# Kernel optimization log

Hardware: AMD Instinct MI355X
Metric: run time of the kernel (lower is better)

The kernel has to match this reference:

```python
import jax, jax.numpy as jnp
import numpy as np

HIDDEN = 2048
NUM_HEADS = 32
NUM_KV_HEADS = 8
HEAD_DIM = 64
ROPE_THETA = 10000.0


def _rope_tables(S, dtype=jnp.float32):
    freqs = 1.0 / (ROPE_THETA ** (jnp.arange(0, HEAD_DIM, 2, dtype=jnp.float32) / HEAD_DIM))
    angles = jnp.arange(S, dtype=jnp.float32)[:, None] * freqs[None, :]  # [S, D/2]
    return jnp.cos(angles).astype(dtype), jnp.sin(angles).astype(dtype)


def _apply_rope(x, cos, sin):
    # x: [B, H, S, D] with interleaved even/odd rotation pairs
    xe = x[..., 0::2]
    xo = x[..., 1::2]
    oe = xe * cos - xo * sin
    oo = xe * sin + xo * cos
    return jnp.stack([oe, oo], axis=-1).reshape(x.shape)


def setup_inputs() -> dict:
    key = jax.random.key(0)
    ks = jax.random.split(key, 5)
    scale = 0.02
    return {
        "x": jax.random.normal(ks[0], (2, 2048, HIDDEN), dtype=jnp.float32),
        "wq": jax.random.normal(ks[1], (NUM_HEADS * HEAD_DIM, HIDDEN), dtype=jnp.float32) * scale,
        "wk": jax.random.normal(ks[2], (NUM_KV_HEADS * HEAD_DIM, HIDDEN), dtype=jnp.float32) * scale,
        "wv": jax.random.normal(ks[3], (NUM_KV_HEADS * HEAD_DIM, HIDDEN), dtype=jnp.float32) * scale,
        "wo": jax.random.normal(ks[4], (HIDDEN, NUM_HEADS * HEAD_DIM), dtype=jnp.float32) * scale,
    }


def reference(x, wq, wk, wv, wo):
    B, S, _ = x.shape
    G = NUM_HEADS // NUM_KV_HEADS  # GQA group size

    q = (x @ wq.T).reshape(B, S, NUM_HEADS, HEAD_DIM).transpose(0, 2, 1, 3)      # [B,Hq,S,D]
    k = (x @ wk.T).reshape(B, S, NUM_KV_HEADS, HEAD_DIM).transpose(0, 2, 1, 3)   # [B,Hkv,S,D]
    v = (x @ wv.T).reshape(B, S, NUM_KV_HEADS, HEAD_DIM).transpose(0, 2, 1, 3)

    cos, sin = _rope_tables(S, x.dtype)
    q = _apply_rope(q, cos, sin)
    k = _apply_rope(k, cos, sin)

    # GQA without materializing repeated K/V: fold group dim into q
    qg = q.reshape(B, NUM_KV_HEADS, G, S, HEAD_DIM)
    scale = 1.0 / jnp.sqrt(jnp.asarray(HEAD_DIM, dtype=x.dtype))
    scores = jnp.einsum("bkgsd,bktd->bkgst", qg, k) * scale  # [B,Hkv,G,S,S]

    causal = jnp.tril(jnp.ones((S, S), dtype=bool))
    scores = jnp.where(causal, scores, jnp.finfo(scores.dtype).min)
    probs = jax.nn.softmax(scores, axis=-1)

    out = jnp.einsum("bkgst,bktd->bkgsd", probs, v)                 # [B,Hkv,G,S,D]
    out = out.reshape(B, NUM_HEADS, S, HEAD_DIM).transpose(0, 2, 1, 3).reshape(B, S, NUM_HEADS * HEAD_DIM)
    return out @ wo.T
```

## Files before the change

kernel.cpp:

```cpp
#include <hip/hip_runtime.h>
#include <hip/hip_bf16.h>

typedef __hip_bfloat16 bf16;
typedef __attribute__((ext_vector_type(8))) short short8;
typedef __attribute__((ext_vector_type(4))) float f32x4;

#define S_LEN 2048
#define BATCH 2
#define M_TOT 4096
#define HID 2048
#define NH 32
#define NKV 8
#define HD 64
#define KVD 512
#define QSCALE 0.125f

#define MFMA16(a, b, c) __builtin_amdgcn_mfma_f32_16x16x32_bf16(a, b, c, 0, 0, 0)

__device__ __forceinline__ void gload_lds16(const bf16* g, bf16* l) {
    __builtin_amdgcn_global_load_lds((const __attribute__((address_space(1))) void*)g,
                                     (__attribute__((address_space(3))) void*)l,
                                     16, 0, 0);
}

__device__ __forceinline__ float b2f(short v) {
    unsigned u = ((unsigned)(unsigned short)v) << 16;
    float f; __builtin_memcpy(&f, &u, 4); return f;
}

#define N8_X   1048576
#define N8_WQ   524288
#define N8_WK   131072
#define N8_TOT 2359296
__global__ void cast_all_kernel(const float* __restrict__ x, const float* __restrict__ wq,
                                const float* __restrict__ wk, const float* __restrict__ wv,
                                const float* __restrict__ wo, bf16* __restrict__ dst) {
    int stride = gridDim.x * blockDim.x;
    for (int i = blockIdx.x * blockDim.x + threadIdx.x; i < N8_TOT; i += stride) {
        const float* s; int off;
        if (i < N8_X)                        { s = x;  off = i; }
        else if (i < N8_X + N8_WQ)           { s = wq; off = i - N8_X; }
        else if (i < N8_X + N8_WQ + N8_WK)   { s = wk; off = i - (N8_X + N8_WQ); }
        else if (i < N8_X + N8_WQ + 2*N8_WK) { s = wv; off = i - (N8_X + N8_WQ + N8_WK); }
        else                                 { s = wo; off = i - (N8_X + N8_WQ + 2*N8_WK); }
        const float4* sp = (const float4*)(s + (size_t)off * 8);
        float4 a = sp[0], b = sp[1];
        bf16 tmp[8];
        tmp[0] = __float2bfloat16(a.x); tmp[1] = __float2bfloat16(a.y);
        tmp[2] = __float2bfloat16(a.z); tmp[3] = __float2bfloat16(a.w);
        tmp[4] = __float2bfloat16(b.x); tmp[5] = __float2bfloat16(b.y);
        tmp[6] = __float2bfloat16(b.z); tmp[7] = __float2bfloat16(b.w);
        *(short8*)(dst + (size_t)i * 8) = *(short8*)tmp;
    }
}

__global__ void rope_tables_kernel(float* __restrict__ cosb, float* __restrict__ sinb) {
    int idx = blockIdx.x * blockDim.x + threadIdx.x;
    if (idx >= S_LEN * 32) return;
    int s = idx >> 5, d = idx & 31;
    float freq = powf(10000.0f, -(float)(2 * d) / 64.0f);
    float ang = (float)s * freq;
    cosb[idx] = cosf(ang);
    sinb[idx] = sinf(ang);
}

__device__ __forceinline__ short8 rope8(short8 v, float4 c, float4 s, float scale) {
    short8 o;
    const float* cp = (const float*)&c;
    const float* sp = (const float*)&s;
    #pragma unroll
    for (int m = 0; m < 4; m++) {
        float xe = b2f(v[2 * m]) * scale;
        float xo = b2f(v[2 * m + 1]) * scale;
        bf16 oe = __float2bfloat16(xe * cp[m] - xo * sp[m]);
        bf16 oo = __float2bfloat16(xe * sp[m] + xo * cp[m]);
        short se, so;
        __builtin_memcpy(&se, &oe, 2); __builtin_memcpy(&so, &oo, 2);
        o[2 * m] = se; o[2 * m + 1] = so;
    }
    return o;
}

__device__ __forceinline__ void gemm_core(const bf16* __restrict__ A,
                                          const bf16* __restrict__ W,
                                          int K, int m0, int n0,
                                          bf16* As, bf16* Bs,
                                          f32x4 acc[4][4]) {
    int tid = threadIdx.x;
    int lane = tid & 63, wid = tid >> 6;
    int wr = wid >> 1, wc = wid & 1;
    int lhi = lane >> 4, llo = lane & 15;
    int c0 = tid, c1 = tid + 256;
    int r0 = c0 >> 2, s0 = ((c0 & 3) ^ ((r0 >> 1) & 3)) * 8;
    int r1 = c1 >> 2, s1 = ((c1 & 3) ^ ((r1 >> 1) & 3)) * 8;
    const bf16* gA0 = A + (size_t)(m0 + r0) * K + s0;
    const bf16* gA1 = A + (size_t)(m0 + r1) * K + s1;
    const bf16* gB0 = W + (size_t)(n0 + r0) * K + s0;
    const bf16* gB1 = W + (size_t)(n0 + r1) * K + s1;

    auto stage = [&](int buf, int k0) {
        bf16* a = As + buf * 4096;
        bf16* b = Bs + buf * 4096;
        gload_lds16(gA0 + k0, a + c0 * 8);
        gload_lds16(gA1 + k0, a + c1 * 8);
        gload_lds16(gB0 + k0, b + c0 * 8);
        gload_lds16(gB1 + k0, b + c1 * 8);
    };
    auto compute = [&](int buf) {
        const bf16* Ac = As + buf * 4096;
        const bf16* Bc = Bs + buf * 4096;
        short8 af[4], bfr[4];
        #pragma unroll
        for (int i = 0; i < 4; i++) {
            int row = wr * 64 + i * 16 + llo;
            af[i] = *(const short8*)(Ac + row * 32 + ((lhi ^ ((row >> 1) & 3)) * 8));
        }
        #pragma unroll
        for (int j = 0; j < 4; j++) {
            int row = wc * 64 + j * 16 + llo;
            bfr[j] = *(const short8*)(Bc + row * 32 + ((lhi ^ ((row >> 1) & 3)) * 8));
        }
        __builtin_amdgcn_s_setprio(1);
        #pragma unroll
        for (int i = 0; i < 4; i++)
            #pragma unroll
            for (int j = 0; j < 4; j++)
                acc[i][j] = MFMA16(af[i], bfr[j], acc[i][j]);
        __builtin_amdgcn_s_setprio(0);
    };

    int nt = K / 32;
    stage(0, 0);
    stage(1, 32);
    int b0 = 0, b1 = 1, b2 = 2;
    for (int t = 0; t < nt - 1; ++t) {
        asm volatile("s_waitcnt vmcnt(4)" ::: "memory");
        __builtin_amdgcn_s_barrier();
        if (t + 2 < nt) stage(b2, (t + 2) * 32);
        __builtin_amdgcn_sched_barrier(0);
        compute(b0);
        int tmp = b0; b0 = b1; b1 = b2; b2 = tmp;
    }
    asm volatile("s_waitcnt vmcnt(0)" ::: "memory");
    __builtin_amdgcn_s_barrier();
    compute(b0);
}

__global__ __launch_bounds__(256) void gemm_qkv_kernel(
        const bf16* __restrict__ xb,
        const bf16* __restrict__ wq, const bf16* __restrict__ wk, const bf16* __restrict__ wv,
        const float* __restrict__ cosb, const float* __restrict__ sinb,
        bf16* __restrict__ qb, bf16* __restrict__ kb, bf16* __restrict__ vtb) {
    __shared__ bf16 As[3 * 128 * 32];
    __shared__ bf16 Bs[3 * 128 * 32];
    int by = blockIdx.y;
    const bf16* W; bf16* Cb; int n0, ldc, mode;
    if (by < 16)      { W = wq; Cb = qb;  n0 = by * 128;        ldc = 2048; mode = 0; }
    else if (by < 20) { W = wk; Cb = kb;  n0 = (by - 16) * 128; ldc = 512;  mode = 2; }
    else              { W = wv; Cb = vtb; n0 = (by - 20) * 128; ldc = 0;    mode = 1; }
    int bx = blockIdx.x;
    int bxs = (bx & 7) * 4 + (bx >> 3);
    int m0 = bxs * 128;

    f32x4 acc[4][4] = {};
    gemm_core(xb, W, HID, m0, n0, As, Bs, acc);

    int lane = threadIdx.x & 63, wid = threadIdx.x >> 6;
    int wr = wid >> 1, wc = wid & 1;
    int lhi = lane >> 4, llo = lane & 15;
    #pragma unroll
    for (int i = 0; i < 4; i++)
        #pragma unroll
        for (int j = 0; j < 4; j++) {
            int col = wc * 64 + j * 16 + llo;
            #pragma unroll
            for (int r = 0; r < 4; r++) {
                int row = wr * 64 + i * 16 + lhi * 4 + r;
                int m = m0 + row;
                float v = acc[i][j][r];
                if (mode == 0) {
                    Cb[(size_t)m * ldc + n0 + col] = __float2bfloat16(v);
                } else if (mode == 1) {
                    int bb = m >> 11, ss = m & 2047;
                    Cb[((size_t)(bb * 512 + n0 + col)) * S_LEN + ss] = __float2bfloat16(v);
                } else {
                    int dcol = n0 + col;
                    int dd = dcol & 63;
                    int pidx = dd >> 1;
                    float sgn = (dd & 1) ? 1.0f : -1.0f;
                    int ss = m & 2047;
                    float c  = cosb[ss * 32 + pidx];
                    float sn = sinb[ss * 32 + pidx];
                    float o = __shfl_xor(v, 1, 64);
                    float outv = v * c + sgn * o * sn;
                    Cb[(size_t)m * 512 + dcol] = __float2bfloat16(outv);
                }
            }
        }
}

__global__ __launch_bounds__(256) void gemm_out_kernel(
        const bf16* __restrict__ attnb, const bf16* __restrict__ wob,
        float* __restrict__ out) {
    __shared__ bf16 As[3 * 128 * 32];
    __shared__ bf16 Bs[3 * 128 * 32];
    int bx = blockIdx.x;
    int bxs = (bx & 7) * 4 + (bx >> 3);
    int m0 = bxs * 128;
    int n0 = blockIdx.y * 128;
    f32x4 acc[4][4] = {};
    gemm_core(attnb, wob, HID, m0, n0, As, Bs, acc);

    int lane = threadIdx.x & 63, wid = threadIdx.x >> 6;
    int wr = wid >> 1, wc = wid & 1;
    int lhi = lane >> 4, llo = lane & 15;
    #pragma unroll
    for (int i = 0; i < 4; i++)
        #pragma unroll
        for (int j = 0; j < 4; j++) {
            int col = wc * 64 + j * 16 + llo;
            #pragma unroll
            for (int r = 0; r < 4; r++) {
                int row = wr * 64 + i * 16 + lhi * 4 + r;
                out[(size_t)(m0 + row) * HID + n0 + col] = acc[i][j][r];
            }
        }
}

__global__ __launch_bounds__(256, 4) void flash_kernel(
        const bf16* __restrict__ qb, const bf16* __restrict__ kb,
        const bf16* __restrict__ vtb, const float* __restrict__ cosb,
        const float* __restrict__ sinb, bf16* __restrict__ attnb) {
    __shared__ bf16 Ks[2][64 * 64];
    __shared__ bf16 Vs[2][64 * 64];
    __shared__ bf16 Pl[4][16 * 64];
    int bh = blockIdx.y;
    int b = bh >> 5, h = bh & 31;
    int kvh = h >> 2;
    int tid = threadIdx.x;
    int wid = tid >> 6, lane = tid & 63;
    int lhi = lane >> 4, llo = lane & 15;
    int jA = blockIdx.x, jB = 31 - jA;

    const bf16* Kg = kb + (size_t)(b * S_LEN) * KVD + kvh * HD;
    const bf16* Vg = vtb + (size_t)(b * 512 + kvh * 64) * S_LEN;

    int c0 = tid, c1 = tid + 256;
    int r0 = c0 >> 3, s0 = ((c0 & 7) ^ (r0 & 7)) * 8;
    int r1 = c1 >> 3, s1 = ((c1 & 7) ^ (r1 & 7)) * 8;

    bf16* pl = &Pl[wid][0];
    const int xw = llo & 7;
    const int hh = lhi >> 1;
    bf16* pwb = pl + llo * 64 + (lhi & 1) * 4;
    const int prd0 = llo * 64 + ((lhi ^ xw) * 8);
    const int prd1 = llo * 64 + (((lhi + 4) ^ xw) * 8);

    auto stage = [&](int buf, int t0) {
        gload_lds16(Kg + (size_t)(t0 + r0) * KVD + s0, &Ks[buf][c0 * 8]);
        gload_lds16(Kg + (size_t)(t0 + r1) * KVD + s1, &Ks[buf][c1 * 8]);
        gload_lds16(Vg + (size_t)r0 * S_LEN + t0 + s0, &Vs[buf][c0 * 8]);
        gload_lds16(Vg + (size_t)r1 * S_LEN + t0 + s1, &Vs[buf][c1 * 8]);
    };

    int qrowA0 = jA * 64 + wid * 16;
    int qrowB0 = jB * 64 + wid * 16;
    short8 qfA0, qfA1, qfB0, qfB1;
    {
        int spos = qrowA0 + llo;
        const bf16* qr = qb + ((size_t)(b * S_LEN) + spos) * (NH * HD) + h * HD;
        float4 c0v = *(const float4*)(cosb + spos * 32 + lhi * 4);
        float4 s0v = *(const float4*)(sinb + spos * 32 + lhi * 4);
        float4 c1v = *(const float4*)(cosb + spos * 32 + 16 + lhi * 4);
        float4 s1v = *(const float4*)(sinb + spos * 32 + 16 + lhi * 4);
        qfA0 = rope8(*(const short8*)(qr + lhi * 8), c0v, s0v, QSCALE);
        qfA1 = rope8(*(const short8*)(qr + 32 + lhi * 8), c1v, s1v, QSCALE);
    }
    {
        int spos = qrowB0 + llo;
        const bf16* qr = qb + ((size_t)(b * S_LEN) + spos) * (NH * HD) + h * HD;
        float4 c0v = *(const float4*)(cosb + spos * 32 + lhi * 4);
        float4 s0v = *(const float4*)(sinb + spos * 32 + lhi * 4);
        float4 c1v = *(const float4*)(cosb + spos * 32 + 16 + lhi * 4);
        float4 s1v = *(const float4*)(sinb + spos * 32 + 16 + lhi * 4);
        qfB0 = rope8(*(const short8*)(qr + lhi * 8), c0v, s0v, QSCALE);
        qfB1 = rope8(*(const short8*)(qr + 32 + lhi * 8), c1v, s1v, QSCALE);
    }

    f32x4 accA[4] = {}, accB[4] = {};
    float psumA = 0.f, psumB = 0.f;
    int qloc = wid * 16 + llo;

    stage(0, 0);
    asm volatile("s_waitcnt vmcnt(0)" ::: "memory");
    __builtin_amdgcn_s_barrier();
    int cur = 0;
    for (int t = 0; t <= jB; ++t) {
        int t0 = t * 64;
        if (t < jB) stage(cur ^ 1, t0 + 64);
        const bf16* Kc = &Ks[cur][0];
        const bf16* Vc = &Vs[cur][0];
        bool doA = (t <= jA);
        f32x4 zA[4], zB[4];
        __builtin_amdgcn_s_setprio(1);
        #pragma unroll
        for (int cb = 0; cb < 4; cb++) {
            int row = cb * 16 + llo;
            short8 k0 = *(const short8*)(Kc + row * 64 + ((lhi ^ xw) * 8));
            short8 k1 = *(const short8*)(Kc + row * 64 + (((lhi + 4) ^ xw) * 8));
            f32x4 zz = {0.f, 0.f, 0.f, 0.f};
            zz = MFMA16(k0, qfB0, zz);
            zz = MFMA16(k1, qfB1, zz);
            zB[cb] = zz;
            if (doA) {
                f32x4 yy = {0.f, 0.f, 0.f, 0.f};
                yy = MFMA16(k0, qfA0, yy);
                yy = MFMA16(k1, qfA1, yy);
                zA[cb] = yy;
            }
        }
        __builtin_amdgcn_s_setprio(0);
        if (doA) {
            bool diag = (t == jA);
            #pragma unroll
            for (int cb = 0; cb < 4; cb++) {
                float p0 = __expf(zA[cb][0]);
                float p1 = __expf(zA[cb][1]);
                float p2 = __expf(zA[cb][2]);
                float p3 = __expf(zA[cb][3]);
                if (diag) {
                    int kl = cb * 16 + lhi * 4;
                    p0 = (kl + 0 <= qloc) ? p0 : 0.f;
                    p1 = (kl + 1 <= qloc) ? p1 : 0.f;
                    p2 = (kl + 2 <= qloc) ? p2 : 0.f;
                    p3 = (kl + 3 <= qloc) ? p3 : 0.f;
                }
                psumA += (p0 + p1) + (p2 + p3);
                bf16 tmp[4];
                tmp[0] = __float2bfloat16(p0); tmp[1] = __float2bfloat16(p1);
                tmp[2] = __float2bfloat16(p2); tmp[3] = __float2bfloat16(p3);
                *(uint2*)(pwb + (((2 * cb + hh) ^ xw) * 8)) = *(uint2*)tmp;
            }
            short8 pa0 = *(const short8*)(pl + prd0);
            short8 pa1 = *(const short8*)(pl + prd1);
            __builtin_amdgcn_s_setprio(1);
            #pragma unroll
            for (int jb = 0; jb < 4; jb++) {
                int row = jb * 16 + llo;
                short8 v0 = *(const short8*)(Vc + row * 64 + ((lhi ^ xw) * 8));
                short8 v1 = *(const short8*)(Vc + row * 64 + (((lhi + 4) ^ xw) * 8));
                accA[jb] = MFMA16(pa0, v0, accA[jb]);
                accA[jb] = MFMA16(pa1, v1, accA[jb]);
            }
            __builtin_amdgcn_s_setprio(0);
        }
        {
            bool diag = (t == jB);
            #pragma unroll
            for (int cb = 0; cb < 4; cb++) {
                float p0 = __expf(zB[cb][0]);
                float p1 = __expf(zB[cb][1]);
                float p2 = __expf(zB[cb][2]);
                float p3 = __expf(zB[cb][3]);
                if (diag) {
                    int kl = cb * 16 + lhi * 4;
                    p0 = (kl + 0 <= qloc) ? p0 : 0.f;
                    p1 = (kl + 1 <= qloc) ? p1 : 0.f;
                    p2 = (kl + 2 <= qloc) ? p2 : 0.f;
                    p3 = (kl + 3 <= qloc) ? p3 : 0.f;
                }
                psumB += (p0 + p1) + (p2 + p3);
                bf16 tmp[4];
                tmp[0] = __float2bfloat16(p0); tmp[1] = __float2bfloat16(p1);
                tmp[2] = __float2bfloat16(p2); tmp[3] = __float2bfloat16(p3);
                *(uint2*)(pwb + (((2 * cb + hh) ^ xw) * 8)) = *(uint2*)tmp;
            }
            short8 pb0 = *(const short8*)(pl + prd0);
            short8 pb1 = *(const short8*)(pl + prd1);
            __builtin_amdgcn_s_setprio(1);
            #pragma unroll
            for (int jb = 0; jb < 4; jb++) {
                int row = jb * 16 + llo;
                short8 v0 = *(const short8*)(Vc + row * 64 + ((lhi ^ xw) * 8));
                short8 v1 = *(const short8*)(Vc + row * 64 + (((lhi + 4) ^ xw) * 8));
                accB[jb] = MFMA16(pb0, v0, accB[jb]);
                accB[jb] = MFMA16(pb1, v1, accB[jb]);
            }
            __builtin_amdgcn_s_setprio(0);
        }
        asm volatile("s_waitcnt vmcnt(0)" ::: "memory");
        __builtin_amdgcn_s_barrier();
        cur ^= 1;
    }
    psumA += __shfl_xor(psumA, 16, 64);
    psumA += __shfl_xor(psumA, 32, 64);
    psumB += __shfl_xor(psumB, 16, 64);
    psumB += __shfl_xor(psumB, 32, 64);
    float invA[4], invB[4];
    #pragma unroll
    for (int r = 0; r < 4; r++) {
        invA[r] = 1.0f / __shfl(psumA, lhi * 4 + r, 64);
        invB[r] = 1.0f / __shfl(psumB, lhi * 4 + r, 64);
    }
    size_t obaseA = ((size_t)(b * S_LEN) + qrowA0) * (NH * HD) + h * HD;
    size_t obaseB = ((size_t)(b * S_LEN) + qrowB0) * (NH * HD) + h * HD;
    #pragma unroll
    for (int jb = 0; jb < 4; jb++)
        #pragma unroll
        for (int r = 0; r < 4; r++) {
            int row = lhi * 4 + r;
            attnb[obaseA + (size_t)row * (NH * HD) + jb * 16 + llo] =
                __float2bfloat16(accA[jb][r] * invA[r]);
            attnb[obaseB + (size_t)row * (NH * HD) + jb * 16 + llo] =
                __float2bfloat16(accB[jb][r] * invB[r]);
        }
}

extern "C" void kernel_launch(void* const* d_in, const int* in_sizes, int n_in,
                              void* d_out, int out_size, void* d_ws, size_t ws_size,
                              hipStream_t stream) {
    const float* x  = (const float*)d_in[0];
    const float* wq = (const float*)d_in[1];
    const float* wk = (const float*)d_in[2];
    const float* wv = (const float*)d_in[3];
    const float* wo = (const float*)d_in[4];
    float* out = (float*)d_out;

    char* ws = (char*)d_ws;
    size_t off = 0;
    auto alloc = [&](size_t bytes) { void* p = ws + off; off += (bytes + 255) & ~(size_t)255; return p; };
    bf16* xb   = (bf16*)alloc((size_t)M_TOT * HID * 2);
    bf16* wqb  = (bf16*)alloc((size_t)HID * HID * 2);
    bf16* wkb  = (bf16*)alloc((size_t)512 * HID * 2);
    bf16* wvb  = (bf16*)alloc((size_t)512 * HID * 2);
    bf16* wob  = (bf16*)alloc((size_t)HID * HID * 2);
    bf16* qb   = (bf16*)alloc((size_t)M_TOT * 2048 * 2);
    bf16* kb   = (bf16*)alloc((size_t)M_TOT * 512 * 2);
    bf16* vtb  = (bf16*)alloc((size_t)M_TOT * 512 * 2);
    bf16* attnb= (bf16*)alloc((size_t)M_TOT * 2048 * 2);
    float* cosb= (float*)alloc((size_t)S_LEN * 32 * 4);
    float* sinb= (float*)alloc((size_t)S_LEN * 32 * 4);

    cast_all_kernel<<<2048, 256, 0, stream>>>(x, wq, wk, wv, wo, xb);

    rope_tables_kernel<<<(S_LEN * 32 + 255) / 256, 256, 0, stream>>>(cosb, sinb);

    gemm_qkv_kernel<<<dim3(M_TOT / 128, 24), 256, 0, stream>>>(xb, wqb, wkb, wvb,
                                                               cosb, sinb, qb, kb, vtb);

    flash_kernel<<<dim3(16, BATCH * NH), 256, 0, stream>>>(qb, kb, vtb, cosb, sinb, attnb);

    gemm_out_kernel<<<dim3(M_TOT / 128, HID / 128), 256, 0, stream>>>(attnb, wob, out);
}
```

Baseline: 194.4 us.

## Use 256x256 tile, 512-thread double-buffered GEMM for QKV projection

Replaces the 128x128-tile, 256-thread, triple-buffered QKV GEMM with a dedicated 256x256-tile kernel using 8 waves, BK=64, and double buffering with XOR-swizzled LDS. Each wave computes a 128x64 sub-tile, which raises arithmetic intensity per LDS and global load. The grid drops from 768 blocks to 192, which is fewer than the CU count and can leave CUs idle. LDS use rises to 128KB per block, and the waitcnt(0) barrier per iteration reduces load/compute overlap.

New measurement: 215.6 us. 1.11x slower.

```diff
diff --git a/kernel.cpp b/kernel.cpp
--- a/kernel.cpp
+++ b/kernel.cpp
@@ -81,6 +81,114 @@
     return o;
 }
 
+__global__ __launch_bounds__(512, 2) void gemm_qkv256_kernel(
+        const bf16* __restrict__ xb,
+        const bf16* __restrict__ wq, const bf16* __restrict__ wk, const bf16* __restrict__ wv,
+        const float* __restrict__ cosb, const float* __restrict__ sinb,
+        bf16* __restrict__ qb, bf16* __restrict__ kb, bf16* __restrict__ vtb) {
+    __shared__ bf16 As[2][256 * 64];
+    __shared__ bf16 Bs[2][256 * 64];
+    int tid = threadIdx.x;
+    int lane = tid & 63, w = tid >> 6;
+    int wr = w >> 2, wc = w & 3;
+    int lhi = lane >> 4, llo = lane & 15;
+
+    int by = blockIdx.y;
+    const bf16* W; int n0, mode;
+    if (by < 8)       { W = wq; n0 = by * 256;        mode = 0; }
+    else if (by < 10) { W = wk; n0 = (by - 8) * 256;  mode = 2; }
+    else              { W = wv; n0 = (by - 10) * 256; mode = 1; }
+    int bx = blockIdx.x;
+    int bxs = (bx & 7) * 2 + (bx >> 3);
+    int m0 = bxs * 256;
+
+    const bf16 *gA[4], *gB[4];
+    int dc[4];
+    #pragma unroll
+    for (int q = 0; q < 4; q++) {
+        int c = tid + 512 * q;
+        int row = c >> 3;
+        int sl = (c & 7) ^ (row & 7);
+        gA[q] = xb + (size_t)(m0 + row) * HID + sl * 8;
+        gB[q] = W + (size_t)(n0 + row) * HID + sl * 8;
+        dc[q] = c * 8;
+    }
+    auto stage = [&](int buf, int k0) {
+        #pragma unroll
+        for (int q = 0; q < 4; q++) gload_lds16(gA[q] + k0, &As[buf][dc[q]]);
+        #pragma unroll
+        for (int q = 0; q < 4; q++) gload_lds16(gB[q] + k0, &Bs[buf][dc[q]]);
+    };
+
+    f32x4 acc[8][4] = {};
+
+    stage(0, 0);
+    stage(1, 64);
+    asm volatile("s_waitcnt vmcnt(8)" ::: "memory");
+    __builtin_amdgcn_s_barrier();
+
+    const int nt = HID / 64;
+    for (int t = 0; t < nt; ++t) {
+        int buf = t & 1;
+        const bf16* Ac = &As[buf][0];
+        const bf16* Bc = &Bs[buf][0];
+        short8 bfr[4][2];
+        #pragma unroll
+        for (int j = 0; j < 4; j++) {
+            int row = wc * 64 + j * 16 + llo;
+            int x = row & 7;
+            bfr[j][0] = *(const short8*)(Bc + row * 64 + ((lhi ^ x) * 8));
+            bfr[j][1] = *(const short8*)(Bc + row * 64 + (((4 + lhi) ^ x) * 8));
+        }
+        #pragma unroll
+        for (int i = 0; i < 8; i++) {
+            int row = wr * 128 + i * 16 + llo;
+            int x = row & 7;
+            short8 a0 = *(const short8*)(Ac + row * 64 + ((lhi ^ x) * 8));
+            short8 a1 = *(const short8*)(Ac + row * 64 + (((4 + lhi) ^ x) * 8));
+            __builtin_amdgcn_s_setprio(1);
+            #pragma unroll
+            for (int j = 0; j < 4; j++)
+                acc[i][j] = MFMA16(a0, bfr[j][0], acc[i][j]);
+            #pragma unroll
+            for (int j = 0; j < 4; j++)
+                acc[i][j] = MFMA16(a1, bfr[j][1], acc[i][j]);
+            __builtin_amdgcn_s_setprio(0);
+        }
+        asm volatile("s_waitcnt vmcnt(0)" ::: "memory");
+        __builtin_amdgcn_s_barrier();
+        if (t + 2 < nt) stage(buf, (t + 2) * 64);
+    }
+
+    #pragma unroll
+    for (int i = 0; i < 8; i++)
+        #pragma unroll
+        for (int j = 0; j < 4; j++) {
+            int col = wc * 64 + j * 16 + llo;
+            #pragma unroll
+            for (int r = 0; r < 4; r++) {
+                int m = m0 + wr * 128 + i * 16 + lhi * 4 + r;
+                float v = acc[i][j][r];
+                if (mode == 0) {
+                    qb[(size_t)m * 2048 + n0 + col] = __float2bfloat16(v);
+                } else if (mode == 1) {
+                    int bb = m >> 11, ss = m & 2047;
+                    vtb[((size_t)(bb * 512 + n0 + col)) * S_LEN + ss] = __float2bfloat16(v);
+                } else {
+                    int dcol = n0 + col;
+                    int dd = dcol & 63;
+                    int pidx = dd >> 1;
+                    float sgn = (dd & 1) ? 1.0f : -1.0f;
+                    int ss = m & 2047;
+                    float c  = cosb[ss * 32 + pidx];
+                    float sn = sinb[ss * 32 + pidx];
+                    float o = __shfl_xor(v, 1, 64);
+                    kb[(size_t)m * 512 + dcol] = __float2bfloat16(v * c + sgn * o * sn);
+                }
+            }
+        }
+}
+
 __device__ __forceinline__ void gemm_core(const bf16* __restrict__ A,
                                           const bf16* __restrict__ W,
                                           int K, int m0, int n0,
@@ -144,59 +252,6 @@
     asm volatile("s_waitcnt vmcnt(0)" ::: "memory");
     __builtin_amdgcn_s_barrier();
     compute(b0);
-}
-
-__global__ __launch_bounds__(256) void gemm_qkv_kernel(
-        const bf16* __restrict__ xb,
-        const bf16* __restrict__ wq, const bf16* __restrict__ wk, const bf16* __restrict__ wv,
-        const float* __restrict__ cosb, const float* __restrict__ sinb,
-        bf16* __restrict__ qb, bf16* __restrict__ kb, bf16* __restrict__ vtb) {
-    __shared__ bf16 As[3 * 128 * 32];
-    __shared__ bf16 Bs[3 * 128 * 32];
-    int by = blockIdx.y;
-    const bf16* W; bf16* Cb; int n0, ldc, mode;
-    if (by < 16)      { W = wq; Cb = qb;  n0 = by * 128;        ldc = 2048; mode = 0; }
-    else if (by < 20) { W = wk; Cb = kb;  n0 = (by - 16) * 128; ldc = 512;  mode = 2; }
-    else              { W = wv; Cb = vtb; n0 = (by - 20) * 128; ldc = 0;    mode = 1; }
-    int bx = blockIdx.x;
-    int bxs = (bx & 7) * 4 + (bx >> 3);
-    int m0 = bxs * 128;
-
-    f32x4 acc[4][4] = {};
-    gemm_core(xb, W, HID, m0, n0, As, Bs, acc);
-
-    int lane = threadIdx.x & 63, wid = threadIdx.x >> 6;
-    int wr = wid >> 1, wc = wid & 1;
-    int lhi = lane >> 4, llo = lane & 15;
-    #pragma unroll
-    for (int i = 0; i < 4; i++)
-        #pragma unroll
-        for (int j = 0; j < 4; j++) {
-            int col = wc * 64 + j * 16 + llo;
-            #pragma unroll
-            for (int r = 0; r < 4; r++) {
-                int row = wr * 64 + i * 16 + lhi * 4 + r;
-                int m = m0 + row;
-                float v = acc[i][j][r];
-                if (mode == 0) {
-                    Cb[(size_t)m * ldc + n0 + col] = __float2bfloat16(v);
-                } else if (mode == 1) {
-                    int bb = m >> 11, ss = m & 2047;
-                    Cb[((size_t)(bb * 512 + n0 + col)) * S_LEN + ss] = __float2bfloat16(v);
-                } else {
-                    int dcol = n0 + col;
-                    int dd = dcol & 63;
-                    int pidx = dd >> 1;
-                    float sgn = (dd & 1) ? 1.0f : -1.0f;
-                    int ss = m & 2047;
-                    float c  = cosb[ss * 32 + pidx];
-                    float sn = sinb[ss * 32 + pidx];
-                    float o = __shfl_xor(v, 1, 64);
-                    float outv = v * c + sgn * o * sn;
-                    Cb[(size_t)m * 512 + dcol] = __float2bfloat16(outv);
-                }
-            }
-        }
 }
 
 __global__ __launch_bounds__(256) void gemm_out_kernel(
@@ -445,8 +500,8 @@
 
     rope_tables_kernel<<<(S_LEN * 32 + 255) / 256, 256, 0, stream>>>(cosb, sinb);
 
-    gemm_qkv_kernel<<<dim3(M_TOT / 128, 24), 256, 0, stream>>>(xb, wqb, wkb, wvb,
-                                                               cosb, sinb, qb, kb, vtb);
+    gemm_qkv256_kernel<<<dim3(16, 12), 512, 0, stream>>>(xb, wqb, wkb, wvb,
+                                                         cosb, sinb, qb, kb, vtb);
 
     flash_kernel<<<dim3(16, BATCH * NH), 256, 0, stream>>>(qb, kb, vtb, cosb, sinb, attnb);
 
```
